# Kernel tuning notes

Measured on AMD Instinct MI355X. Metric: run time of the kernel, lower is better.

The kernel has to match this reference:

```python
import jax, jax.numpy as jnp
import numpy as np

B, C, H, W = 64, 64, 56, 56
MID = 2 * C  # two output nodes concatenated
EPS = 1e-5


def _conv1x1(x, w):
    # x: [B,C,H,W], w: [O,C] (1x1 conv kernel squeezed)
    return jnp.einsum('bchw,oc->bohw', x, w)


def _bn(x, g, b, m, v):
    # eval-mode BatchNorm2d with running stats
    sc = g * jax.lax.rsqrt(v + EPS)
    return x * sc[None, :, None, None] + (b - m * sc)[None, :, None, None]


def _maxpool3(x):
    # MaxPool2d(kernel=3, stride=1, padding=1)
    return jax.lax.reduce_window(x, -jnp.inf, jax.lax.max,
                                 (1, 1, 3, 3), (1, 1, 1, 1),
                                 [(0, 0), (0, 0), (1, 1), (1, 1)])


def _avgpool3(x):
    # AvgPool2d(kernel=3, stride=1, padding=1), count_include_pad=True -> /9
    s = jax.lax.reduce_window(x, 0.0, jax.lax.add,
                              (1, 1, 3, 3), (1, 1, 1, 1),
                              [(0, 0), (0, 0), (1, 1), (1, 1)])
    return s * (1.0 / 9.0)


def setup_inputs() -> dict:
    key = jax.random.key(0)
    ks = jax.random.split(key, 11)
    x = jax.random.normal(ks[0], (B, C, H, W), dtype=jnp.float32)
    w1 = jax.random.normal(ks[1], (C, C), dtype=jnp.float32) * 0.1
    w2 = jax.random.normal(ks[2], (C, MID), dtype=jnp.float32) * 0.1
    bn1_g = 1.0 + 0.1 * jax.random.normal(ks[3], (C,), dtype=jnp.float32)
    bn1_b = 0.1 * jax.random.normal(ks[4], (C,), dtype=jnp.float32)
    bn1_m = 0.1 * jax.random.normal(ks[5], (C,), dtype=jnp.float32)
    bn1_v = jax.random.uniform(ks[6], (C,), minval=0.5, maxval=1.5, dtype=jnp.float32)
    bn2_g = 1.0 + 0.1 * jax.random.normal(ks[7], (C,), dtype=jnp.float32)
    bn2_b = 0.1 * jax.random.normal(ks[8], (C,), dtype=jnp.float32)
    bn2_m = 0.1 * jax.random.normal(ks[9], (C,), dtype=jnp.float32)
    bn2_v = jax.random.uniform(ks[10], (C,), minval=0.5, maxval=1.5, dtype=jnp.float32)
    return dict(x=x, w1=w1, w2=w2,
                bn1_g=bn1_g, bn1_b=bn1_b, bn1_m=bn1_m, bn1_v=bn1_v,
                bn2_g=bn2_g, bn2_b=bn2_b, bn2_m=bn2_m, bn2_v=bn2_v)


def reference(x, w1, w2, bn1_g, bn1_b, bn1_m, bn1_v, bn2_g, bn2_b, bn2_m, bn2_v):
    # DAG g = [[[0,1],[1,2]], [[4,3],[3]], [[5,3],[3,100]], [[4,3],[100]]]
    # topoSort order: [0, 2, 1, 3]; output nodes (ordered): [2, 3]
    node0 = jax.nn.relu(_bn(_conv1x1(x, w1), bn1_g, bn1_b, bn1_m, bn1_v))
    node1 = _maxpool3(node0)            # op type 4, pred {0}
    node2 = _avgpool3(node0)            # op type 5, pred {0}
    node3 = _maxpool3(node1) + _maxpool3(node2)  # op type 4, preds {1,2}, summed
    cat = jnp.concatenate([node2, node3], axis=1)  # [B, 2C, H, W]
    out = jax.nn.relu(_bn(_conv1x1(cat, w2), bn2_g, bn2_b, bn2_m, bn2_v))
    return out
```

## Files before the change

kernel.cpp:

```cpp
#include <hip/hip_runtime.h>
#include <cstddef>

#define EPS 1e-5f
static constexpr int Bn = 64, Cn = 64, Hn = 56, Wn = 56, HWn = Hn * Wn;
static constexpr int XS = 65;

typedef __attribute__((ext_vector_type(8))) short short8;
typedef __attribute__((ext_vector_type(8))) unsigned short ushort8;
typedef __attribute__((ext_vector_type(4))) float floatx4;
typedef __attribute__((ext_vector_type(16))) float floatx16;
typedef __attribute__((ext_vector_type(4))) unsigned int uintx4;
typedef __attribute__((ext_vector_type(2))) unsigned int uintx2;

__device__ __forceinline__ unsigned pack_rne(float a, float b) {
    unsigned ua = __float_as_uint(a), ub = __float_as_uint(b);
    ua = ua + 0x7fffu + ((ua >> 16) & 1u);
    ub = ub + 0x7fffu + ((ub >> 16) & 1u);
    return __builtin_amdgcn_perm(ub, ua, 0x07060302);
}
__device__ __forceinline__ unsigned pack_trunc(float a, float b) {
    return __builtin_amdgcn_perm(__float_as_uint(b), __float_as_uint(a), 0x07060302);
}
__device__ __forceinline__ ushort8 pmax(ushort8 a, ushort8 b) {
    return __builtin_elementwise_max(a, b);
}
__device__ __forceinline__ float bf_lo(unsigned u) { return __uint_as_float(u << 16); }
__device__ __forceinline__ float bf_hi(unsigned u) { return __uint_as_float(u & 0xffff0000u); }


__global__ __launch_bounds__(256) void k1_conv1(
    const float* __restrict__ x, const float* __restrict__ w1,
    const float* __restrict__ bg, const float* __restrict__ bb,
    const float* __restrict__ bm, const float* __restrict__ bv,
    unsigned short* __restrict__ node0)
{
    __shared__ float xs[2][64 * XS];
    __shared__ float scs[64], shs[64];
    const int tid = threadIdx.x;
    if (tid < 64) {
        float sc = bg[tid] * rsqrtf(bv[tid] + EPS);
        scs[tid] = sc;
        shs[tid] = bb[tid] - bm[tid] * sc;
    }
    __syncthreads();
    const int lane = tid & 63;
    const int wv   = tid >> 6;
    const int m    = lane & 15;
    const int quad = lane >> 4;
    const int qoff = quad * 8;

    short8 afr[4][2];
    float shv[16];
    #pragma unroll
    for (int t = 0; t < 4; ++t) {
        const float sc = scs[t * 16 + m];
        #pragma unroll
        for (int kk = 0; kk < 2; ++kk) {
            const float* wp = w1 + (t * 16 + m) * 64 + kk * 32 + qoff;
            floatx4 f0 = *(const floatx4*)wp;
            floatx4 f1 = *(const floatx4*)(wp + 4);
            uintx4 u;
            u.x = pack_rne(f0[0] * sc, f0[1] * sc);
            u.y = pack_rne(f0[2] * sc, f0[3] * sc);
            u.z = pack_rne(f1[0] * sc, f1[1] * sc);
            u.w = pack_rne(f1[2] * sc, f1[3] * sc);
            afr[t][kk] = *(short8*)&u;
        }
        #pragma unroll
        for (int i = 0; i < 4; ++i) shv[t * 4 + i] = shs[t * 16 + quad * 4 + i];
    }

    floatx4 stg[4];
    auto ldtile = [&](int tt) {
        const int P = blockIdx.x * 256 + tt * 64;
        const int b = P / HWn, p0 = P - b * HWn;
        #pragma unroll
        for (int q = 0; q < 4; ++q) {
            int idx = q * 256 + tid;
            int c = idx >> 4, f = idx & 15;
            stg[q] = *(const floatx4*)(x + (size_t)(b * 64 + c) * HWn + p0 + f * 4);
        }
    };
    auto sttile = [&](int buf) {
        #pragma unroll
        for (int q = 0; q < 4; ++q) {
            int idx = q * 256 + tid;
            int c = idx >> 4, f = idx & 15;
            #pragma unroll
            for (int k = 0; k < 4; ++k)
                xs[buf][(f * 4 + k) * XS + c] = stg[q][k];
        }
    };

    ldtile(0);
    sttile(0);

    #pragma unroll
    for (int tt = 0; tt < 4; ++tt) {
        __syncthreads();
        if (tt < 3) ldtile(tt + 1);

        const int P = blockIdx.x * 256 + tt * 64;
        const int b = P / HWn, p0 = P - b * HWn;
        const float* xr = &xs[tt & 1][(wv * 16 + m) * XS];

        floatx4 acc[4];
        #pragma unroll
        for (int t = 0; t < 4; ++t) acc[t] = (floatx4){0.f, 0.f, 0.f, 0.f};

        #pragma unroll
        for (int kk = 0; kk < 2; ++kk) {
            float f[8];
            #pragma unroll
            for (int j = 0; j < 8; ++j) f[j] = xr[kk * 32 + qoff + j];
            uintx4 u;
            u.x = pack_trunc(f[0], f[1]);
            u.y = pack_trunc(f[2], f[3]);
            u.z = pack_trunc(f[4], f[5]);
            u.w = pack_trunc(f[6], f[7]);
            short8 bfr = *(short8*)&u;
            #pragma unroll
            for (int t = 0; t < 4; ++t)
                acc[t] = __builtin_amdgcn_mfma_f32_16x16x32_bf16(afr[t][kk], bfr, acc[t], 0, 0, 0);
        }

        const int chunkbase = (quad >> 1);
        const int j0 = (quad & 1) * 4;
        #pragma unroll
        for (int t = 0; t < 4; ++t) {
            float v0 = acc[t][0] + shv[t * 4 + 0]; v0 = v0 > 0.f ? v0 : 0.f;
            float v1 = acc[t][1] + shv[t * 4 + 1]; v1 = v1 > 0.f ? v1 : 0.f;
            float v2 = acc[t][2] + shv[t * 4 + 2]; v2 = v2 > 0.f ? v2 : 0.f;
            float v3 = acc[t][3] + shv[t * 4 + 3]; v3 = v3 > 0.f ? v3 : 0.f;
            uintx2 st;
            st.x = pack_rne(v0, v1);
            st.y = pack_rne(v2, v3);
            int chunk = t * 2 + chunkbase;
            *(uintx2*)(node0 + ((size_t)(b * 8 + chunk) * HWn + p0 + wv * 16 + m) * 8 + j0) = st;
        }

        if (tt < 3) sttile((tt + 1) & 1);
    }
}

__global__ __launch_bounds__(256) void k2_pools(
    const unsigned short* __restrict__ node0, unsigned short* __restrict__ cat)
{
    const int tid = threadIdx.x;
    const int lane = tid & 63;
    const int wv = tid >> 6;
    const int bid = blockIdx.x;
    const int half = bid & 1;
    const int band = (bid >> 1) % 7;
    const int b = bid / 14;
    const int chunk = half * 4 + wv;
    const int lo = band * 8;
    const int col = lane;
    const bool act = col < Wn;
    const unsigned short* base = node0 + ((size_t)(b * 8 + chunk) * HWn) * 8;
    unsigned short* cavg = cat + ((size_t)(b * 16 + chunk) * HWn) * 8;
    unsigned short* cmax = cat + ((size_t)(b * 16 + 8 + chunk) * HWn) * 8;

    const ushort8 zz = (ushort8)0;
    auto load5 = [&](int r, ushort8* d) {
        #pragma unroll
        for (int dd = 0; dd < 5; ++dd) {
            int cc = col + dd - 2;
            bool ok = act && ((unsigned)cc < (unsigned)Wn) && ((unsigned)r < (unsigned)Hn);
            d[dd] = ok ? *(const ushort8*)(base + (size_t)(r * Wn + cc) * 8) : zz;
        }
    };

    float hs1[8], hs2[8];
    ushort8 h5a = zz, h5b = zz, h5c = zz, h5d = zz, nh1 = zz, nh2 = zz;
    #pragma unroll
    for (int j = 0; j < 8; ++j) hs1[j] = hs2[j] = 0.f;

    ushort8 d[5];
    load5(lo - 2, d);

    #pragma unroll
    for (int i = 0; i < 12; ++i) {
        const int r = lo - 2 + i;
        ushort8 dn[5];
        if (i < 11) load5(r + 1, dn);

        ushort8 hm5 = pmax(pmax(pmax(d[0], d[1]), pmax(d[2], d[3])), d[4]);
        ushort8 m5 = pmax(pmax(pmax(h5a, h5b), pmax(h5c, h5d)), hm5);
        h5a = h5b; h5b = h5c; h5c = h5d; h5d = hm5;

        const uintx4 ul = *(const uintx4*)&d[1];
        const uintx4 uv = *(const uintx4*)&d[2];
        const uintx4 ur = *(const uintx4*)&d[3];
        float a2[8];
        const int r2 = r - 1, r3 = r - 2;
        const bool v2 = (unsigned)r2 < (unsigned)Hn;
        #pragma unroll
        for (int w = 0; w < 4; ++w) {
            float hsum0 = bf_lo(ul[w]) + bf_lo(uv[w]) + bf_lo(ur[w]);
            float hsum1 = bf_hi(ul[w]) + bf_hi(uv[w]) + bf_hi(ur[w]);
            a2[w * 2 + 0] = v2 ? (hs2[w * 2 + 0] + hs1[w * 2 + 0] + hsum0) * (1.f / 9.f) : 0.f;
            a2[w * 2 + 1] = v2 ? (hs2[w * 2 + 1] + hs1[w * 2 + 1] + hsum1) * (1.f / 9.f) : 0.f;
            hs2[w * 2 + 0] = hs1[w * 2 + 0]; hs1[w * 2 + 0] = hsum0;
            hs2[w * 2 + 1] = hs1[w * 2 + 1]; hs1[w * 2 + 1] = hsum1;
        }
        uintx4 ap;
        ap.x = pack_rne(a2[0], a2[1]);
        ap.y = pack_rne(a2[2], a2[3]);
        ap.z = pack_rne(a2[4], a2[5]);
        ap.w = pack_rne(a2[6], a2[7]);
        uintx4 al, ar;
        #pragma unroll
        for (int w = 0; w < 4; ++w) {
            unsigned u = ap[w];
            unsigned lu = __shfl_up(u, 1);
            unsigned ru = __shfl_down(u, 1);
            al[w] = (lane == 0) ? 0u : lu;
            ar[w] = (lane == 63) ? 0u : ru;
        }
        ushort8 nh = pmax(pmax(*(ushort8*)&al, *(ushort8*)&ap), *(ushort8*)&ar);
        ushort8 m3 = pmax(pmax(nh2, nh1), nh);
        nh2 = nh1; nh1 = nh;

        if (act && r2 >= lo && r2 < lo + 8)
            *(uintx4*)(cavg + (size_t)(r2 * Wn + col) * 8) = ap;
        if (act && r3 >= lo && r3 < lo + 8) {
            const uintx4 u5 = *(const uintx4*)&m5;
            const uintx4 u3 = *(const uintx4*)&m3;
            uintx4 st;
            #pragma unroll
            for (int w = 0; w < 4; ++w)
                st[w] = pack_rne(bf_lo(u5[w]) + bf_lo(u3[w]), bf_hi(u5[w]) + bf_hi(u3[w]));
            *(uintx4*)(cmax + (size_t)(r3 * Wn + col) * 8) = st;
        }
        #pragma unroll
        for (int dd = 0; dd < 5; ++dd) d[dd] = dn[dd];
    }
}

__global__ __launch_bounds__(256) void k3_conv2(
    const unsigned short* __restrict__ cat, const float* __restrict__ w2,
    const float* __restrict__ bg, const float* __restrict__ bb,
    const float* __restrict__ bm, const float* __restrict__ bv,
    float* __restrict__ out)
{
    __shared__ unsigned short wl[1024 * 8];
    __shared__ float scs[64], shs[64];
    const int tid = threadIdx.x;
    if (tid < 64) {
        float sc = bg[tid] * rsqrtf(bv[tid] + EPS);
        scs[tid] = sc;
        shs[tid] = bb[tid] - bm[tid] * sc;
    }
    #pragma unroll
    for (int q = 0; q < 4; ++q) {
        int ci = tid * 4 + q;
        int lane_ = ci & 63, tk = ci >> 6;
        int t = tk >> 3, kt = tk & 7, n_ = lane_ & 31, h_ = lane_ >> 5;
        const float* wp = w2 + (t * 32 + n_) * 128 + kt * 16 + h_ * 8;
        floatx4 f0 = *(const floatx4*)wp;
        floatx4 f1 = *(const floatx4*)(wp + 4);
        uintx4 u;
        u.x = pack_rne(f0[0], f0[1]);
        u.y = pack_rne(f0[2], f0[3]);
        u.z = pack_rne(f1[0], f1[1]);
        u.w = pack_rne(f1[2], f1[3]);
        *(uintx4*)(wl + (size_t)ci * 8) = u;
    }
    __syncthreads();

    const int lane = tid & 63;
    const int wv = tid >> 6;
    const int n = lane & 31;
    const int h = lane >> 5;

    short8 afr[2][8];
    #pragma unroll
    for (int t = 0; t < 2; ++t)
        #pragma unroll
        for (int kt = 0; kt < 8; ++kt)
            afr[t][kt] = *(const short8*)(wl + ((size_t)((t * 8 + kt) * 64 + lane)) * 8);

    #pragma unroll
    for (int s = 0; s < 2; ++s) {
        const int tile = (blockIdx.x * 4 + wv) * 2 + s;
        const int b = tile / 98;
        const int p0 = (tile - b * 98) * 32;

        floatx16 acc0, acc1;
        #pragma unroll
        for (int i = 0; i < 16; ++i) { acc0[i] = 0.f; acc1[i] = 0.f; }

        #pragma unroll
        for (int kt = 0; kt < 8; ++kt) {
            short8 bfr = *(const short8*)(cat + ((size_t)(b * 16 + kt * 2 + h) * HWn + p0 + n) * 8);
            acc0 = __builtin_amdgcn_mfma_f32_32x32x16_bf16(afr[0][kt], bfr, acc0, 0, 0, 0);
            acc1 = __builtin_amdgcn_mfma_f32_32x32x16_bf16(afr[1][kt], bfr, acc1, 0, 0, 0);
        }

        float* ob = out + (size_t)b * 64 * HWn + p0 + n;
        #pragma unroll
        for (int r = 0; r < 16; ++r) {
            int o = (r & 3) + 8 * (r >> 2) + 4 * h;
            float v0 = fmaf(acc0[r], scs[o], shs[o]);
            ob[(size_t)o * HWn] = v0 > 0.f ? v0 : 0.f;
            float v1 = fmaf(acc1[r], scs[o + 32], shs[o + 32]);
            ob[(size_t)(o + 32) * HWn] = v1 > 0.f ? v1 : 0.f;
        }
    }
}

extern "C" void kernel_launch(void* const* d_in, const int* in_sizes, int n_in,
                              void* d_out, int out_size, void* d_ws, size_t ws_size,
                              hipStream_t stream)
{
    const float* x   = (const float*)d_in[0];
    const float* w1  = (const float*)d_in[1];
    const float* w2  = (const float*)d_in[2];
    const float* b1g = (const float*)d_in[3];
    const float* b1b = (const float*)d_in[4];
    const float* b1m = (const float*)d_in[5];
    const float* b1v = (const float*)d_in[6];
    const float* b2g = (const float*)d_in[7];
    const float* b2b = (const float*)d_in[8];
    const float* b2m = (const float*)d_in[9];
    const float* b2v = (const float*)d_in[10];

    float* out = (float*)d_out;
    unsigned short* node0 = (unsigned short*)d_ws;
    unsigned short* cat   = node0 + (size_t)Bn * HWn * 64;

    k1_conv1<<<dim3(784), dim3(256), 0, stream>>>(x, w1, b1g, b1b, b1m, b1v, node0);
    k2_pools<<<dim3(Bn * 14), dim3(256), 0, stream>>>(node0, cat);
    k3_conv2<<<dim3(784), dim3(256), 0, stream>>>(cat, w2, b2g, b2b, b2m, b2v, out);
}
```

Measured before the change: 159.9 us.

## Halve per-block work in pools and conv2, add nontemporal IO, pack float2 math

The pooling kernel now covers 4-row bands instead of 8, doubling its grid, and the second conv kernel handles one tile per wave instead of two, also doubling its grid. Input loads in conv1 and output stores in conv2 become nontemporal, and the avgpool arithmetic is rewritten with float2 vectors so the compiler can use packed ops. The smaller pool bands increase halo reloads (8 rows loaded per 4 output rows instead of 12 per 8), and the smaller conv2 blocks repeat the weight staging more often per output.

```diff
diff --git a/kernel.cpp b/kernel.cpp
--- a/kernel.cpp
+++ b/kernel.cpp
@@ -7,6 +7,7 @@
 
 typedef __attribute__((ext_vector_type(8))) short short8;
 typedef __attribute__((ext_vector_type(8))) unsigned short ushort8;
+typedef __attribute__((ext_vector_type(2))) float floatx2;
 typedef __attribute__((ext_vector_type(4))) float floatx4;
 typedef __attribute__((ext_vector_type(16))) float floatx16;
 typedef __attribute__((ext_vector_type(4))) unsigned int uintx4;
@@ -26,6 +27,9 @@
 }
 __device__ __forceinline__ float bf_lo(unsigned u) { return __uint_as_float(u << 16); }
 __device__ __forceinline__ float bf_hi(unsigned u) { return __uint_as_float(u & 0xffff0000u); }
+__device__ __forceinline__ floatx2 bf2(unsigned u) {
+    floatx2 f; f.x = bf_lo(u); f.y = bf_hi(u); return f;
+}
 
 
 __global__ __launch_bounds__(256) void k1_conv1(
@@ -78,7 +82,8 @@
         for (int q = 0; q < 4; ++q) {
             int idx = q * 256 + tid;
             int c = idx >> 4, f = idx & 15;
-            stg[q] = *(const floatx4*)(x + (size_t)(b * 64 + c) * HWn + p0 + f * 4);
+            stg[q] = __builtin_nontemporal_load(
+                (const floatx4*)(x + (size_t)(b * 64 + c) * HWn + p0 + f * 4));
         }
     };
     auto sttile = [&](int buf) {
@@ -151,10 +156,10 @@
     const int wv = tid >> 6;
     const int bid = blockIdx.x;
     const int half = bid & 1;
-    const int band = (bid >> 1) % 7;
-    const int b = bid / 14;
+    const int band = (bid >> 1) % 14;
+    const int b = bid / 28;
     const int chunk = half * 4 + wv;
-    const int lo = band * 8;
+    const int lo = band * 4;
     const int col = lane;
     const bool act = col < Wn;
     const unsigned short* base = node0 + ((size_t)(b * 8 + chunk) * HWn) * 8;
@@ -171,19 +176,19 @@
         }
     };
 
-    float hs1[8], hs2[8];
+    floatx2 hs1[4], hs2[4];
     ushort8 h5a = zz, h5b = zz, h5c = zz, h5d = zz, nh1 = zz, nh2 = zz;
     #pragma unroll
-    for (int j = 0; j < 8; ++j) hs1[j] = hs2[j] = 0.f;
+    for (int j = 0; j < 4; ++j) { hs1[j] = (floatx2){0.f, 0.f}; hs2[j] = (floatx2){0.f, 0.f}; }
 
     ushort8 d[5];
     load5(lo - 2, d);
 
     #pragma unroll
-    for (int i = 0; i < 12; ++i) {
+    for (int i = 0; i < 8; ++i) {
         const int r = lo - 2 + i;
         ushort8 dn[5];
-        if (i < 11) load5(r + 1, dn);
+        if (i < 7) load5(r + 1, dn);
 
         ushort8 hm5 = pmax(pmax(pmax(d[0], d[1]), pmax(d[2], d[3])), d[4]);
         ushort8 m5 = pmax(pmax(pmax(h5a, h5b), pmax(h5c, h5d)), hm5);
@@ -192,23 +197,21 @@
         const uintx4 ul = *(const uintx4*)&d[1];
         const uintx4 uv = *(const uintx4*)&d[2];
         const uintx4 ur = *(const uintx4*)&d[3];
-        float a2[8];
         const int r2 = r - 1, r3 = r - 2;
         const bool v2 = (unsigned)r2 < (unsigned)Hn;
+        const float mul9 = v2 ? (1.f / 9.f) : 0.f;
+        floatx2 a2[4];
         #pragma unroll
         for (int w = 0; w < 4; ++w) {
-            float hsum0 = bf_lo(ul[w]) + bf_lo(uv[w]) + bf_lo(ur[w]);
-            float hsum1 = bf_hi(ul[w]) + bf_hi(uv[w]) + bf_hi(ur[w]);
-            a2[w * 2 + 0] = v2 ? (hs2[w * 2 + 0] + hs1[w * 2 + 0] + hsum0) * (1.f / 9.f) : 0.f;
-            a2[w * 2 + 1] = v2 ? (hs2[w * 2 + 1] + hs1[w * 2 + 1] + hsum1) * (1.f / 9.f) : 0.f;
-            hs2[w * 2 + 0] = hs1[w * 2 + 0]; hs1[w * 2 + 0] = hsum0;
-            hs2[w * 2 + 1] = hs1[w * 2 + 1]; hs1[w * 2 + 1] = hsum1;
+            floatx2 hsum = bf2(ul[w]) + bf2(uv[w]) + bf2(ur[w]);
+            a2[w] = (hs2[w] + hs1[w] + hsum) * mul9;
+            hs2[w] = hs1[w]; hs1[w] = hsum;
         }
         uintx4 ap;
-        ap.x = pack_rne(a2[0], a2[1]);
-        ap.y = pack_rne(a2[2], a2[3]);
-        ap.z = pack_rne(a2[4], a2[5]);
-        ap.w = pack_rne(a2[6], a2[7]);
+        ap.x = pack_rne(a2[0].x, a2[0].y);
+        ap.y = pack_rne(a2[1].x, a2[1].y);
+        ap.z = pack_rne(a2[2].x, a2[2].y);
+        ap.w = pack_rne(a2[3].x, a2[3].y);
         uintx4 al, ar;
         #pragma unroll
         for (int w = 0; w < 4; ++w) {
@@ -222,15 +225,17 @@
         ushort8 m3 = pmax(pmax(nh2, nh1), nh);
         nh2 = nh1; nh1 = nh;
 
-        if (act && r2 >= lo && r2 < lo + 8)
+        if (act && r2 >= lo && r2 < lo + 4)
             *(uintx4*)(cavg + (size_t)(r2 * Wn + col) * 8) = ap;
-        if (act && r3 >= lo && r3 < lo + 8) {
+        if (act && r3 >= lo && r3 < lo + 4) {
             const uintx4 u5 = *(const uintx4*)&m5;
             const uintx4 u3 = *(const uintx4*)&m3;
             uintx4 st;
             #pragma unroll
-            for (int w = 0; w < 4; ++w)
-                st[w] = pack_rne(bf_lo(u5[w]) + bf_lo(u3[w]), bf_hi(u5[w]) + bf_hi(u3[w]));
+            for (int w = 0; w < 4; ++w) {
+                floatx2 sm = bf2(u5[w]) + bf2(u3[w]);
+                st[w] = pack_rne(sm.x, sm.y);
+            }
             *(uintx4*)(cmax + (size_t)(r3 * Wn + col) * 8) = st;
         }
         #pragma unroll
@@ -281,32 +286,29 @@
         for (int kt = 0; kt < 8; ++kt)
             afr[t][kt] = *(const short8*)(wl + ((size_t)((t * 8 + kt) * 64 + lane)) * 8);
 
-    #pragma unroll
-    for (int s = 0; s < 2; ++s) {
-        const int tile = (blockIdx.x * 4 + wv) * 2 + s;
-        const int b = tile / 98;
-        const int p0 = (tile - b * 98) * 32;
-
-        floatx16 acc0, acc1;
-        #pragma unroll
-        for (int i = 0; i < 16; ++i) { acc0[i] = 0.f; acc1[i] = 0.f; }
-
-        #pragma unroll
-        for (int kt = 0; kt < 8; ++kt) {
-            short8 bfr = *(const short8*)(cat + ((size_t)(b * 16 + kt * 2 + h) * HWn + p0 + n) * 8);
-            acc0 = __builtin_amdgcn_mfma_f32_32x32x16_bf16(afr[0][kt], bfr, acc0, 0, 0, 0);
-            acc1 = __builtin_amdgcn_mfma_f32_32x32x16_bf16(afr[1][kt], bfr, acc1, 0, 0, 0);
-        }
-
-        float* ob = out + (size_t)b * 64 * HWn + p0 + n;
-        #pragma unroll
-        for (int r = 0; r < 16; ++r) {
-            int o = (r & 3) + 8 * (r >> 2) + 4 * h;
-            float v0 = fmaf(acc0[r], scs[o], shs[o]);
-            ob[(size_t)o * HWn] = v0 > 0.f ? v0 : 0.f;
-            float v1 = fmaf(acc1[r], scs[o + 32], shs[o + 32]);
-            ob[(size_t)(o + 32) * HWn] = v1 > 0.f ? v1 : 0.f;
-        }
+    const int tile = blockIdx.x * 4 + wv;
+    const int b = tile / 98;
+    const int p0 = (tile - b * 98) * 32;
+
+    floatx16 acc0, acc1;
+    #pragma unroll
+    for (int i = 0; i < 16; ++i) { acc0[i] = 0.f; acc1[i] = 0.f; }
+
+    #pragma unroll
+    for (int kt = 0; kt < 8; ++kt) {
+        short8 bfr = *(const short8*)(cat + ((size_t)(b * 16 + kt * 2 + h) * HWn + p0 + n) * 8);
+        acc0 = __builtin_amdgcn_mfma_f32_32x32x16_bf16(afr[0][kt], bfr, acc0, 0, 0, 0);
+        acc1 = __builtin_amdgcn_mfma_f32_32x32x16_bf16(afr[1][kt], bfr, acc1, 0, 0, 0);
+    }
+
+    float* ob = out + (size_t)b * 64 * HWn + p0 + n;
+    #pragma unroll
+    for (int r = 0; r < 16; ++r) {
+        int o = (r & 3) + 8 * (r >> 2) + 4 * h;
+        float v0 = fmaf(acc0[r], scs[o], shs[o]);
+        __builtin_nontemporal_store(v0 > 0.f ? v0 : 0.f, ob + (size_t)o * HWn);
+        float v1 = fmaf(acc1[r], scs[o + 32], shs[o + 32]);
+        __builtin_nontemporal_store(v1 > 0.f ? v1 : 0.f, ob + (size_t)(o + 32) * HWn);
     }
 }
 
@@ -331,6 +333,6 @@
     unsigned short* cat   = node0 + (size_t)Bn * HWn * 64;
 
     k1_conv1<<<dim3(784), dim3(256), 0, stream>>>(x, w1, b1g, b1b, b1m, b1v, node0);
-    k2_pools<<<dim3(Bn * 14), dim3(256), 0, stream>>>(node0, cat);
-    k3_conv2<<<dim3(784), dim3(256), 0, stream>>>(cat, w2, b2g, b2b, b2m, b2v, out);
-}
+    k2_pools<<<dim3(Bn * 28), dim3(256), 0, stream>>>(node0, cat);
+    k3_conv2<<<dim3(1568), dim3(256), 0, stream>>>(cat, w2, b2g, b2b, b2m, b2v, out);
+}
```

After: 165.5 us. 3.5% more time.
